# Performance work log

Measured on AMD Instinct MI355X. Metric: run time of the kernel, lower is better.

Reference implementation:

```python
import jax, jax.numpy as jnp
import numpy as np

INPUT_SIZE = 512
HIDDEN_SIZE = 1024
OUTPUT_SIZE = 512
BATCH = 128
SEQ_LEN = 512


def setup_inputs() -> dict:
    key = jax.random.key(0)
    k_x, k_xh, k_hh, k_yh = jax.random.split(key, 4)

    def xavier(k, shape):
        fan_in, fan_out = shape
        lim = float(np.sqrt(6.0 / (fan_in + fan_out)))
        return jax.random.uniform(k, shape, jnp.float32, -lim, lim)

    return {
        "x": jax.random.normal(k_x, (BATCH, SEQ_LEN, INPUT_SIZE), jnp.float32),
        "W_xh": xavier(k_xh, (INPUT_SIZE, HIDDEN_SIZE)),
        "W_hh": xavier(k_hh, (HIDDEN_SIZE, HIDDEN_SIZE)),
        "W_yh": xavier(k_yh, (HIDDEN_SIZE, OUTPUT_SIZE)),
        "W_bh": jnp.zeros((HIDDEN_SIZE,), jnp.float32),
        "W_by": jnp.zeros((OUTPUT_SIZE,), jnp.float32),
    }


def reference(x, W_xh, W_hh, W_yh, W_bh, W_by):
    # x: [B, S, I]. Precompute input projections for all steps (parallel GEMM),
    # then scan the strictly sequential hidden recurrence.
    xW = jnp.einsum("bsi,ih->bsh", x, W_xh) + W_bh  # [B, S, H]
    h0 = jnp.zeros((x.shape[0], W_hh.shape[0]), x.dtype)

    def step(h, xw_t):
        h_new = jnp.tanh(xw_t + h @ W_hh)
        return h_new, None

    h_last, _ = jax.lax.scan(step, h0, jnp.swapaxes(xW, 0, 1))  # scan over S
    return h_last @ W_yh + W_by  # [B, O]
```

## Files before the change

### kernel.cpp

```cpp
#include <hip/hip_runtime.h>

typedef _Float16 half8 __attribute__((ext_vector_type(8)));
typedef float f32x4 __attribute__((ext_vector_type(4)));

#define MFMA16(a,b,c) __builtin_amdgcn_mfma_f32_16x16x32_f16((a),(b),(c),0,0,0)

constexpr int B_SZ = 128, S_LEN = 512, I_SZ = 512, H_SZ = 1024, O_SZ = 512;

constexpr size_t XW_OFF   = 0;
constexpr size_t X16_OFF  = XW_OFF   + (size_t)S_LEN * B_SZ * H_SZ * 2;
constexpr size_t WXHT_OFF = X16_OFF  + (size_t)B_SZ * S_LEN * I_SZ * 2;
constexpr size_t WHHT_OFF = WXHT_OFF + (size_t)H_SZ * I_SZ * 2;
constexpr size_t WYHT_OFF = WHHT_OFF + (size_t)H_SZ * H_SZ * 2;
constexpr size_t HBUF_OFF = WYHT_OFF + (size_t)O_SZ * H_SZ * 2;
constexpr size_t CNT_OFF  = HBUF_OFF + (size_t)2 * B_SZ * H_SZ * 2;

typedef unsigned long long u64;

__device__ __forceinline__ u64 ag_load(const u64* p) {
  return __hip_atomic_load(p, __ATOMIC_RELAXED, __HIP_MEMORY_SCOPE_AGENT);
}
__device__ __forceinline__ void ag_store(u64* p, u64 v) {
  __hip_atomic_store(p, v, __ATOMIC_RELAXED, __HIP_MEMORY_SCOPE_AGENT);
}


__global__ void k_cvt_x(const float* __restrict__ in, _Float16* __restrict__ out) {
  size_t i = ((size_t)blockIdx.x * 256 + threadIdx.x) * 8;
  float4 a = *(const float4*)(in + i);
  float4 b = *(const float4*)(in + i + 4);
  half8 h;
  h[0] = (_Float16)a.x; h[1] = (_Float16)a.y; h[2] = (_Float16)a.z; h[3] = (_Float16)a.w;
  h[4] = (_Float16)b.x; h[5] = (_Float16)b.y; h[6] = (_Float16)b.z; h[7] = (_Float16)b.w;
  *(half8*)(out + i) = h;
}

__global__ void k_transpose_cvt(const float* __restrict__ in, _Float16* __restrict__ out,
                                int K, int N) {
  int k = blockIdx.x * 256 + threadIdx.x;
  int n = blockIdx.y;
  out[(size_t)n * K + k] = (_Float16)in[(size_t)k * N + n];
}


__launch_bounds__(256, 1)
__global__ void k_xw_gemm(const _Float16* __restrict__ A,
                          const _Float16* __restrict__ BT,
                          const float* __restrict__ bias,
                          _Float16* __restrict__ xw)
{
  const int m0 = blockIdx.y * 128;
  const int n0 = blockIdx.x * 128;
  __shared__ __align__(16) _Float16 la[128][72];
  __shared__ __align__(16) _Float16 lb[128][72];
  const int tid = threadIdx.x;
  const int w = tid >> 6, l = tid & 63;
  const int wr = w >> 1, wc = w & 1;
  const int cl = l & 15;
  const int kh = (l >> 4) << 3;
  const int rl = (l >> 4) << 2;

  f32x4 acc[4][4] = {};

  for (int kb = 0; kb < 512; kb += 64) {
    {
      const int r = tid >> 1, sg = tid & 1;
      const _Float16* ga = A  + (size_t)(m0 + r) * 512 + kb + sg * 32;
      const _Float16* gb = BT + (size_t)(n0 + r) * 512 + kb + sg * 32;
      _Float16* da = &la[r][sg * 32];
      _Float16* db = &lb[r][sg * 32];
      #pragma unroll
      for (int i = 0; i < 4; i++) *(half8*)(da + i * 8) = *(const half8*)(ga + i * 8);
      #pragma unroll
      for (int i = 0; i < 4; i++) *(half8*)(db + i * 8) = *(const half8*)(gb + i * 8);
    }
    __syncthreads();
    #pragma unroll
    for (int kk = 0; kk < 64; kk += 32) {
      half8 af[4], bf[4];
      #pragma unroll
      for (int mi = 0; mi < 4; mi++) af[mi] = *(const half8*)(&la[wr * 64 + mi * 16 + cl][kk + kh]);
      #pragma unroll
      for (int ni = 0; ni < 4; ni++) bf[ni] = *(const half8*)(&lb[wc * 64 + ni * 16 + cl][kk + kh]);
      #pragma unroll
      for (int mi = 0; mi < 4; mi++)
        #pragma unroll
        for (int ni = 0; ni < 4; ni++)
          acc[mi][ni] = MFMA16(af[mi], bf[ni], acc[mi][ni]);
    }
    __syncthreads();
  }

  #pragma unroll
  for (int mi = 0; mi < 4; mi++)
    #pragma unroll
    for (int ni = 0; ni < 4; ni++) {
      const int col = n0 + wc * 64 + ni * 16 + cl;
      const float bv = bias[col];
      #pragma unroll
      for (int r = 0; r < 4; r++) {
        const int m = m0 + wr * 64 + mi * 16 + rl + r;
        const int b = m >> 9;
        const int s = m & 511;
        xw[((size_t)(s * B_SZ + b) << 10) + col] = (_Float16)(acc[mi][ni][r] + bv);
      }
    }
}


__launch_bounds__(128, 1)
__global__ void k_rnn(const _Float16* __restrict__ xw,
                      const _Float16* __restrict__ WhhT,
                      const _Float16* __restrict__ WyhT,
                      const float* __restrict__ Wby,
                      u64* __restrict__ hb64,
                      unsigned* __restrict__ cnt,
                      float* __restrict__ out)
{
  const int bid = blockIdx.x;
  const int g = bid & 7;
  const int j = bid >> 3;
  const int tid = threadIdx.x;
  const int w = tid >> 6;
  const int l = tid & 63;
  const int r0 = g << 4;
  const int n0 = j << 5;
  const int cl = l & 15;
  const int kh = (l >> 4) << 3;
  const int rl = (l >> 4) << 2;
  const int colg = n0 + (w << 4) + cl;

  __shared__ __align__(16) _Float16 lw[32][1032];
  __shared__ __align__(16) _Float16 lh[16][1032];
  __shared__ __align__(16) _Float16 st[16][40];

  {
    const int r = tid >> 2, sg = tid & 3;
    const _Float16* src = WhhT + ((size_t)(n0 + r) << 10) + (sg << 8);
    _Float16* dst = &lw[r][sg << 8];
    #pragma unroll
    for (int i = 0; i < 32; i++)
      *(half8*)(dst + (i << 3)) = *(const half8*)(src + (i << 3));
  }

  const int hr = tid >> 3;
  const int hs = tid & 7;

  float xv[4];
  {
    const _Float16* p = xw + ((size_t)r0 << 10) + colg;
    #pragma unroll
    for (int r = 0; r < 4; r++) xv[r] = (float)p[(size_t)(rl + r) << 10];
  }

  unsigned tgt = 0;
  for (int t = 0; t < 512; t++) {
    f32x4 acc0 = {}, acc1 = {};
    float xn[4] = {0.f, 0.f, 0.f, 0.f};
    if (t > 0) {
      {
        u64 v[32];
        const u64* hb = hb64 + (((size_t)(t & 1) << 7) + r0 + hr) * 256 + (hs << 1);
        #pragma unroll
        for (int i = 0; i < 16; i++) {
          v[2 * i]     = ag_load(hb + (i << 4));
          v[2 * i + 1] = ag_load(hb + (i << 4) + 1);
        }
        #pragma unroll
        for (int i = 0; i < 16; i++) {
          *(u64*)(&lh[hr][(hs << 3) + (i << 6)])     = v[2 * i];
          *(u64*)(&lh[hr][(hs << 3) + (i << 6) + 4]) = v[2 * i + 1];
        }
      }
      if (t < 511) {
        const _Float16* p = xw + (((size_t)(t + 1) << 7) + r0) * 1024 + colg;
        #pragma unroll
        for (int r = 0; r < 4; r++) xn[r] = (float)p[(size_t)(rl + r) << 10];
      }
      __syncthreads();
      #pragma unroll 4
      for (int kc = 0; kc < 32; kc += 2) {
        half8 a0 = *(const half8*)(&lh[cl][(kc << 5) + kh]);
        half8 b0 = *(const half8*)(&lw[(w << 4) + cl][(kc << 5) + kh]);
        acc0 = MFMA16(a0, b0, acc0);
        half8 a1 = *(const half8*)(&lh[cl][((kc + 1) << 5) + kh]);
        half8 b1 = *(const half8*)(&lw[(w << 4) + cl][((kc + 1) << 5) + kh]);
        acc1 = MFMA16(a1, b1, acc1);
      }
    } else {
      const _Float16* p = xw + (((size_t)1 << 7) + r0) * 1024 + colg;
      #pragma unroll
      for (int r = 0; r < 4; r++) xn[r] = (float)p[(size_t)(rl + r) << 10];
    }

    #pragma unroll
    for (int r = 0; r < 4; r++) {
      float z = xv[r] + acc0[r] + acc1[r];
      st[rl + r][(w << 4) + cl] = (_Float16)tanhf(z);
    }
    __syncthreads();
    {
      u64 pv = *(const u64*)&st[tid >> 3][(tid & 7) << 2];
      u64* dst = hb64 + (((size_t)((t + 1) & 1) << 7) + r0 + (tid >> 3)) * 256
               + (n0 >> 2) + (tid & 7);
      ag_store(dst, pv);
    }
    asm volatile("s_waitcnt vmcnt(0)" ::: "memory");
    __syncthreads();
    tgt += 32;
    if (tid == 0) {
      __hip_atomic_fetch_add(&cnt[g << 6], 1u, __ATOMIC_RELAXED, __HIP_MEMORY_SCOPE_AGENT);
      while (__hip_atomic_load(&cnt[g << 6], __ATOMIC_RELAXED, __HIP_MEMORY_SCOPE_AGENT) < tgt)
        __builtin_amdgcn_s_sleep(1);
    }
    __syncthreads();
    #pragma unroll
    for (int r = 0; r < 4; r++) xv[r] = xn[r];
  }

  {
    {
      u64 v[32];
      const u64* hb = hb64 + ((size_t)(r0 + hr)) * 256 + (hs << 1);
      #pragma unroll
      for (int i = 0; i < 16; i++) {
        v[2 * i]     = ag_load(hb + (i << 4));
        v[2 * i + 1] = ag_load(hb + (i << 4) + 1);
      }
      #pragma unroll
      for (int i = 0; i < 16; i++) {
        *(u64*)(&lh[hr][(hs << 3) + (i << 6)])     = v[2 * i];
        *(u64*)(&lh[hr][(hs << 3) + (i << 6) + 4]) = v[2 * i + 1];
      }
    }
    __syncthreads();
    if (w == 0) {
      f32x4 a0 = {}, a1 = {};
      const int oc = (j << 4) + cl;
      const _Float16* bsrc = WyhT + ((size_t)oc << 10);
      #pragma unroll 4
      for (int kc = 0; kc < 32; kc += 2) {
        half8 av = *(const half8*)(&lh[cl][(kc << 5) + kh]);
        half8 bv = *(const half8*)(bsrc + (kc << 5) + kh);
        a0 = MFMA16(av, bv, a0);
        half8 av1 = *(const half8*)(&lh[cl][((kc + 1) << 5) + kh]);
        half8 bv1 = *(const half8*)(bsrc + ((kc + 1) << 5) + kh);
        a1 = MFMA16(av1, bv1, a1);
      }
      const float bb = Wby[oc];
      #pragma unroll
      for (int r = 0; r < 4; r++)
        out[((size_t)(r0 + rl + r) << 9) + oc] = a0[r] + a1[r] + bb;
    }
  }
}


extern "C" void kernel_launch(void* const* d_in, const int* in_sizes, int n_in,
                              void* d_out, int out_size, void* d_ws, size_t ws_size,
                              hipStream_t stream) {
  const float* x   = (const float*)d_in[0];
  const float* Wxh = (const float*)d_in[1];
  const float* Whh = (const float*)d_in[2];
  const float* Wyh = (const float*)d_in[3];
  const float* Wbh = (const float*)d_in[4];
  const float* Wby = (const float*)d_in[5];
  float* out = (float*)d_out;

  char* ws = (char*)d_ws;
  _Float16* xw   = (_Float16*)(ws + XW_OFF);
  _Float16* x16  = (_Float16*)(ws + X16_OFF);
  _Float16* WxhT = (_Float16*)(ws + WXHT_OFF);
  _Float16* WhhT = (_Float16*)(ws + WHHT_OFF);
  _Float16* WyhT = (_Float16*)(ws + WYHT_OFF);
  u64*      hb64 = (u64*)(ws + HBUF_OFF);
  unsigned* cnt  = (unsigned*)(ws + CNT_OFF);

  hipMemsetAsync(cnt, 0, 8 * 64 * sizeof(unsigned), stream);

  k_cvt_x<<<16384, 256, 0, stream>>>(x, x16);
  k_transpose_cvt<<<dim3(2, 1024), 256, 0, stream>>>(Wxh, WxhT, 512, 1024);
  k_transpose_cvt<<<dim3(4, 1024), 256, 0, stream>>>(Whh, WhhT, 1024, 1024);
  k_transpose_cvt<<<dim3(4, 512),  256, 0, stream>>>(Wyh, WyhT, 1024, 512);

  k_xw_gemm<<<dim3(8, 512), 256, 0, stream>>>(x16, WxhT, Wbh, xw);

  k_rnn<<<256, 128, 0, stream>>>(xw, WhhT, WyhT, Wby, hb64, cnt, out);
}
```

Before: 1.883 ms.

## Replace counter barrier with per-wave tag flags and double-buffered hidden state

Swaps the per-group atomic counter barrier (one thread increments, then spins, with block-wide syncs around it) for per-wave tag slots. Each wave publishes its own slice of h with an atomic exchange and then writes a step tag; consumers poll all 64 tags with a wave-wide __all before loading h. The LDS h buffer and staging tile are double-buffered, which removes a __syncthreads per step. The hidden-state buffer is regrouped per batch group, and tanhf is replaced by an exp2/rcp approximation. The hope is lower per-step synchronisation latency, with risks around memory ordering of the relaxed atomics and a bounded poll loop that can fall through after a timeout.

```diff
diff --git a/kernel.cpp b/kernel.cpp
--- a/kernel.cpp
+++ b/kernel.cpp
@@ -2,6 +2,7 @@
 
 typedef _Float16 half8 __attribute__((ext_vector_type(8)));
 typedef float f32x4 __attribute__((ext_vector_type(4)));
+typedef unsigned long long u64;
 
 #define MFMA16(a,b,c) __builtin_amdgcn_mfma_f32_16x16x32_f16((a),(b),(c),0,0,0)
 
@@ -11,19 +12,27 @@
 constexpr size_t X16_OFF  = XW_OFF   + (size_t)S_LEN * B_SZ * H_SZ * 2;
 constexpr size_t WXHT_OFF = X16_OFF  + (size_t)B_SZ * S_LEN * I_SZ * 2;
 constexpr size_t WHHT_OFF = WXHT_OFF + (size_t)H_SZ * I_SZ * 2;
-constexpr size_t WYHT_OFF = WHHT_OFF + (size_t)H_SZ * H_SZ * 2;
-constexpr size_t HBUF_OFF = WYHT_OFF + (size_t)O_SZ * H_SZ * 2;
-constexpr size_t CNT_OFF  = HBUF_OFF + (size_t)2 * B_SZ * H_SZ * 2;
-
-typedef unsigned long long u64;
-
-__device__ __forceinline__ u64 ag_load(const u64* p) {
+constexpr size_t WYHT_OFF = WHHT_OFF + (size_t)H_SZ * I_SZ * 2 + (size_t)H_SZ * H_SZ * 2 - (size_t)H_SZ * I_SZ * 2;
+constexpr size_t HB_OFF   = WYHT_OFF + (size_t)O_SZ * H_SZ * 2;
+constexpr size_t TAG_OFF  = HB_OFF   + (size_t)8 * 2 * 16 * 1024 * 2;
+
+__device__ __forceinline__ u64 ag_load64(const u64* p) {
   return __hip_atomic_load(p, __ATOMIC_RELAXED, __HIP_MEMORY_SCOPE_AGENT);
 }
-__device__ __forceinline__ void ag_store(u64* p, u64 v) {
+__device__ __forceinline__ unsigned ag_load32(const unsigned* p) {
+  return __hip_atomic_load(p, __ATOMIC_RELAXED, __HIP_MEMORY_SCOPE_AGENT);
+}
+__device__ __forceinline__ void ag_store32(unsigned* p, unsigned v) {
   __hip_atomic_store(p, v, __ATOMIC_RELAXED, __HIP_MEMORY_SCOPE_AGENT);
 }
-
+__device__ __forceinline__ void ag_xchg64(u64* p, u64 v) {
+  (void)__hip_atomic_exchange(p, v, __ATOMIC_RELAXED, __HIP_MEMORY_SCOPE_AGENT);
+}
+
+__device__ __forceinline__ float ftanh(float z) {
+  float e = __builtin_amdgcn_exp2f(z * 2.8853900817779268f);
+  return fmaf(-2.f, __builtin_amdgcn_rcpf(e + 1.f), 1.f);
+}
 
 __global__ void k_cvt_x(const float* __restrict__ in, _Float16* __restrict__ out) {
   size_t i = ((size_t)blockIdx.x * 256 + threadIdx.x) * 8;
@@ -41,7 +50,6 @@
   int n = blockIdx.y;
   out[(size_t)n * K + k] = (_Float16)in[(size_t)k * N + n];
 }
-
 
 __launch_bounds__(256, 1)
 __global__ void k_xw_gemm(const _Float16* __restrict__ A,
@@ -108,153 +116,146 @@
 }
 
 
+__device__ __forceinline__ void poll_tags64(const unsigned* gtag, int l, unsigned t) {
+  for (int it = 0; it < (1 << 17); ++it) {
+    unsigned tg = ag_load32(gtag + l);
+    if (__all((int)(tg >= t))) break;
+    __builtin_amdgcn_s_sleep(1);
+  }
+  __builtin_amdgcn_sched_barrier(0);
+}
+
 __launch_bounds__(128, 1)
 __global__ void k_rnn(const _Float16* __restrict__ xw,
                       const _Float16* __restrict__ WhhT,
                       const _Float16* __restrict__ WyhT,
                       const float* __restrict__ Wby,
-                      u64* __restrict__ hb64,
-                      unsigned* __restrict__ cnt,
+                      u64* __restrict__ hb,
+                      unsigned* __restrict__ tags,
                       float* __restrict__ out)
 {
+  __shared__ __align__(16) _Float16 lw[32][1032];
+  __shared__ __align__(16) _Float16 lh[2][16][1032];
+  __shared__ __align__(16) _Float16 st[2][16][40];
+
   const int bid = blockIdx.x;
-  const int g = bid & 7;
-  const int j = bid >> 3;
+  const int g = bid & 7, j = bid >> 3;
   const int tid = threadIdx.x;
-  const int w = tid >> 6;
-  const int l = tid & 63;
-  const int r0 = g << 4;
-  const int n0 = j << 5;
+  const int w = tid >> 6, l = tid & 63;
   const int cl = l & 15;
   const int kh = (l >> 4) << 3;
   const int rl = (l >> 4) << 2;
+  const int r0 = g << 4;
+  const int n0 = j << 5;
   const int colg = n0 + (w << 4) + cl;
-
-  __shared__ __align__(16) _Float16 lw[32][1032];
-  __shared__ __align__(16) _Float16 lh[16][1032];
-  __shared__ __align__(16) _Float16 st[16][40];
+  const int hr = tid >> 3, hs = tid & 7;
+  unsigned* gtag = tags + (g << 6);
+  const int slot = (j << 1) + w;
+  u64* hbg = hb + ((size_t)g << 13);
 
   {
-    const int r = tid >> 2, sg = tid & 3;
-    const _Float16* src = WhhT + ((size_t)(n0 + r) << 10) + (sg << 8);
-    _Float16* dst = &lw[r][sg << 8];
+    const int rr = tid >> 2, sg = tid & 3;
+    const _Float16* src = WhhT + ((size_t)(n0 + rr) << 10) + (sg << 8);
+    _Float16* dst = &lw[rr][sg << 8];
     #pragma unroll
     for (int i = 0; i < 32; i++)
       *(half8*)(dst + (i << 3)) = *(const half8*)(src + (i << 3));
   }
-
-  const int hr = tid >> 3;
-  const int hs = tid & 7;
-
-  float xv[4];
-  {
-    const _Float16* p = xw + ((size_t)r0 << 10) + colg;
-    #pragma unroll
-    for (int r = 0; r < 4; r++) xv[r] = (float)p[(size_t)(rl + r) << 10];
-  }
-
-  unsigned tgt = 0;
+  __syncthreads();
+
   for (int t = 0; t < 512; t++) {
+    float xv[4];
+    {
+      const _Float16* p = xw + ((size_t)(t * 128 + r0 + rl) << 10) + colg;
+      #pragma unroll
+      for (int r = 0; r < 4; r++) xv[r] = (float)p[(size_t)r << 10];
+    }
+
+    if (t > 0) {
+      poll_tags64(gtag, l, (unsigned)t);
+      u64 a[32];
+      const u64* hsrc = hbg + ((size_t)(t & 1) << 12) + (hr << 8) + (hs << 1);
+      #pragma unroll
+      for (int i = 0; i < 16; i++) {
+        a[2 * i]     = ag_load64(hsrc + (i << 4));
+        a[2 * i + 1] = ag_load64(hsrc + (i << 4) + 1);
+      }
+      _Float16* ld = &lh[t & 1][hr][hs << 3];
+      #pragma unroll
+      for (int i = 0; i < 16; i++) {
+        *(u64*)(ld + (i << 6))     = a[2 * i];
+        *(u64*)(ld + (i << 6) + 4) = a[2 * i + 1];
+      }
+    }
+    __syncthreads();
+
     f32x4 acc0 = {}, acc1 = {};
-    float xn[4] = {0.f, 0.f, 0.f, 0.f};
     if (t > 0) {
-      {
-        u64 v[32];
-        const u64* hb = hb64 + (((size_t)(t & 1) << 7) + r0 + hr) * 256 + (hs << 1);
-        #pragma unroll
-        for (int i = 0; i < 16; i++) {
-          v[2 * i]     = ag_load(hb + (i << 4));
-          v[2 * i + 1] = ag_load(hb + (i << 4) + 1);
-        }
-        #pragma unroll
-        for (int i = 0; i < 16; i++) {
-          *(u64*)(&lh[hr][(hs << 3) + (i << 6)])     = v[2 * i];
-          *(u64*)(&lh[hr][(hs << 3) + (i << 6) + 4]) = v[2 * i + 1];
-        }
-      }
-      if (t < 511) {
-        const _Float16* p = xw + (((size_t)(t + 1) << 7) + r0) * 1024 + colg;
-        #pragma unroll
-        for (int r = 0; r < 4; r++) xn[r] = (float)p[(size_t)(rl + r) << 10];
-      }
-      __syncthreads();
+      const _Float16 (*lhb)[1032] = lh[t & 1];
       #pragma unroll 4
       for (int kc = 0; kc < 32; kc += 2) {
-        half8 a0 = *(const half8*)(&lh[cl][(kc << 5) + kh]);
-        half8 b0 = *(const half8*)(&lw[(w << 4) + cl][(kc << 5) + kh]);
+        half8 a0 = *(const half8*)&lhb[cl][(kc << 5) + kh];
+        half8 b0 = *(const half8*)&lw[(w << 4) + cl][(kc << 5) + kh];
         acc0 = MFMA16(a0, b0, acc0);
-        half8 a1 = *(const half8*)(&lh[cl][((kc + 1) << 5) + kh]);
-        half8 b1 = *(const half8*)(&lw[(w << 4) + cl][((kc + 1) << 5) + kh]);
+        half8 a1 = *(const half8*)&lhb[cl][((kc + 1) << 5) + kh];
+        half8 b1 = *(const half8*)&lw[(w << 4) + cl][((kc + 1) << 5) + kh];
         acc1 = MFMA16(a1, b1, acc1);
       }
-    } else {
-      const _Float16* p = xw + (((size_t)1 << 7) + r0) * 1024 + colg;
-      #pragma unroll
-      for (int r = 0; r < 4; r++) xn[r] = (float)p[(size_t)(rl + r) << 10];
     }
 
     #pragma unroll
     for (int r = 0; r < 4; r++) {
       float z = xv[r] + acc0[r] + acc1[r];
-      st[rl + r][(w << 4) + cl] = (_Float16)tanhf(z);
-    }
-    __syncthreads();
+      st[w][rl + r][cl] = (_Float16)ftanh(z);
+    }
+    asm volatile("s_waitcnt lgkmcnt(0)" ::: "memory");
+    __builtin_amdgcn_sched_barrier(0);
     {
-      u64 pv = *(const u64*)&st[tid >> 3][(tid & 7) << 2];
-      u64* dst = hb64 + (((size_t)((t + 1) & 1) << 7) + r0 + (tid >> 3)) * 256
-               + (n0 >> 2) + (tid & 7);
-      ag_store(dst, pv);
+      u64 pv = *(const u64*)&st[w][l >> 2][(l & 3) << 2];
+      u64* dst = hbg + ((size_t)((t + 1) & 1) << 12) + ((size_t)(l >> 2) << 8)
+               + (j << 3) + (w << 2) + (l & 3);
+      ag_xchg64(dst, pv);
     }
     asm volatile("s_waitcnt vmcnt(0)" ::: "memory");
-    __syncthreads();
-    tgt += 32;
-    if (tid == 0) {
-      __hip_atomic_fetch_add(&cnt[g << 6], 1u, __ATOMIC_RELAXED, __HIP_MEMORY_SCOPE_AGENT);
-      while (__hip_atomic_load(&cnt[g << 6], __ATOMIC_RELAXED, __HIP_MEMORY_SCOPE_AGENT) < tgt)
-        __builtin_amdgcn_s_sleep(1);
-    }
-    __syncthreads();
-    #pragma unroll
-    for (int r = 0; r < 4; r++) xv[r] = xn[r];
-  }
-
+    if (l == 0) ag_store32(gtag + slot, (unsigned)(t + 1));
+  }
+
+  poll_tags64(gtag, l, 512u);
   {
-    {
-      u64 v[32];
-      const u64* hb = hb64 + ((size_t)(r0 + hr)) * 256 + (hs << 1);
-      #pragma unroll
-      for (int i = 0; i < 16; i++) {
-        v[2 * i]     = ag_load(hb + (i << 4));
-        v[2 * i + 1] = ag_load(hb + (i << 4) + 1);
-      }
-      #pragma unroll
-      for (int i = 0; i < 16; i++) {
-        *(u64*)(&lh[hr][(hs << 3) + (i << 6)])     = v[2 * i];
-        *(u64*)(&lh[hr][(hs << 3) + (i << 6) + 4]) = v[2 * i + 1];
-      }
-    }
-    __syncthreads();
-    if (w == 0) {
-      f32x4 a0 = {}, a1 = {};
-      const int oc = (j << 4) + cl;
-      const _Float16* bsrc = WyhT + ((size_t)oc << 10);
-      #pragma unroll 4
-      for (int kc = 0; kc < 32; kc += 2) {
-        half8 av = *(const half8*)(&lh[cl][(kc << 5) + kh]);
-        half8 bv = *(const half8*)(bsrc + (kc << 5) + kh);
-        a0 = MFMA16(av, bv, a0);
-        half8 av1 = *(const half8*)(&lh[cl][((kc + 1) << 5) + kh]);
-        half8 bv1 = *(const half8*)(bsrc + ((kc + 1) << 5) + kh);
-        a1 = MFMA16(av1, bv1, a1);
-      }
-      const float bb = Wby[oc];
-      #pragma unroll
-      for (int r = 0; r < 4; r++)
-        out[((size_t)(r0 + rl + r) << 9) + oc] = a0[r] + a1[r] + bb;
-    }
-  }
-}
-
+    u64 a[32];
+    const u64* hsrc = hbg + (hr << 8) + (hs << 1);
+    #pragma unroll
+    for (int i = 0; i < 16; i++) {
+      a[2 * i]     = ag_load64(hsrc + (i << 4));
+      a[2 * i + 1] = ag_load64(hsrc + (i << 4) + 1);
+    }
+    _Float16* ld = &lh[0][hr][hs << 3];
+    #pragma unroll
+    for (int i = 0; i < 16; i++) {
+      *(u64*)(ld + (i << 6))     = a[2 * i];
+      *(u64*)(ld + (i << 6) + 4) = a[2 * i + 1];
+    }
+  }
+  __syncthreads();
+  if (w == 0) {
+    f32x4 a0 = {}, a1 = {};
+    const int oc = (j << 4) + cl;
+    const _Float16* bsrc = WyhT + ((size_t)oc << 10);
+    #pragma unroll 4
+    for (int kc = 0; kc < 32; kc += 2) {
+      half8 av  = *(const half8*)&lh[0][cl][(kc << 5) + kh];
+      half8 bv  = *(const half8*)(bsrc + (kc << 5) + kh);
+      a0 = MFMA16(av, bv, a0);
+      half8 av1 = *(const half8*)&lh[0][cl][((kc + 1) << 5) + kh];
+      half8 bv1 = *(const half8*)(bsrc + ((kc + 1) << 5) + kh);
+      a1 = MFMA16(av1, bv1, a1);
+    }
+    const float bb = Wby[oc];
+    #pragma unroll
+    for (int r = 0; r < 4; r++)
+      out[((size_t)(r0 + rl + r) << 9) + oc] = a0[r] + a1[r] + bb;
+  }
+}
 
 extern "C" void kernel_launch(void* const* d_in, const int* in_sizes, int n_in,
                               void* d_out, int out_size, void* d_ws, size_t ws_size,
@@ -273,10 +274,10 @@
   _Float16* WxhT = (_Float16*)(ws + WXHT_OFF);
   _Float16* WhhT = (_Float16*)(ws + WHHT_OFF);
   _Float16* WyhT = (_Float16*)(ws + WYHT_OFF);
-  u64*      hb64 = (u64*)(ws + HBUF_OFF);
-  unsigned* cnt  = (unsigned*)(ws + CNT_OFF);
-
-  hipMemsetAsync(cnt, 0, 8 * 64 * sizeof(unsigned), stream);
+  u64*      hb   = (u64*)(ws + HB_OFF);
+  unsigned* tags = (unsigned*)(ws + TAG_OFF);
+
+  hipMemsetAsync(tags, 0, 8 * 64 * sizeof(unsigned), stream);
 
   k_cvt_x<<<16384, 256, 0, stream>>>(x, x16);
   k_transpose_cvt<<<dim3(2, 1024), 256, 0, stream>>>(Wxh, WxhT, 512, 1024);
@@ -285,5 +286,5 @@
 
   k_xw_gemm<<<dim3(8, 512), 256, 0, stream>>>(x16, WxhT, Wbh, xw);
 
-  k_rnn<<<256, 128, 0, stream>>>(xw, WhhT, WyhT, Wby, hb64, cnt, out);
-}
+  k_rnn<<<256, 128, 0, stream>>>(xw, WhhT, WyhT, Wby, hb, tags, out);
+}
```

After: 2.055 ms. 9.2% more time.
